# Performance work log

Measured on AMD Instinct MI355X. Metric: run time of the kernel, lower is better.

The kernel has to match this reference:

```python
import jax, jax.numpy as jnp
import numpy as np

N_ENT, N_REL, N_TRIG, N_ARGS = 100000, 250000, 50000, 250000
ENT_DIM, REL_R, RTYPE_DIM, ROLE_DIM, REL_SIZE = 288, 256, 32, 256, 200
ARG_DIM = REL_R + RTYPE_DIM + ENT_DIM  # 576


def setup_inputs() -> dict:
    key = jax.random.key(0)
    ks = jax.random.split(key, 11)
    s_in = 1.0 / np.sqrt(ARG_DIM)
    return {
        "ent_embeds": jax.random.normal(ks[0], (N_ENT, ENT_DIM), jnp.float32),
        "rel_embeds": jax.random.normal(ks[1], (N_REL, REL_R), jnp.float32),
        "rtype_table": jax.random.normal(ks[2], (REL_SIZE + 1, RTYPE_DIM), jnp.float32),
        "W_in": jax.random.normal(ks[3], (ARG_DIM, ROLE_DIM), jnp.float32) * s_in,
        "W_out": jax.random.normal(ks[4], (ARG_DIM, ROLE_DIM), jnp.float32) * s_in,
        "rtype_ids": jax.random.randint(ks[5], (N_REL,), 0, REL_SIZE, jnp.int32),
        "trig_ent_id": jax.random.randint(ks[6], (N_TRIG,), 0, N_ENT, jnp.int32),
        "arg_trig": jax.random.randint(ks[7], (N_ARGS,), 0, N_TRIG, jnp.int32),
        "arg_rel": jax.random.randint(ks[8], (N_ARGS,), 0, N_REL, jnp.int32),
        "arg_ent": jax.random.randint(ks[9], (N_ARGS,), 0, N_ENT, jnp.int32),
        "arg_is_in": jax.random.randint(ks[10], (N_ARGS,), 0, 2, jnp.int32),
    }


def reference(ent_embeds, rel_embeds, rtype_table, W_in, W_out,
              rtype_ids, trig_ent_id, arg_trig, arg_rel, arg_ent, arg_is_in):
    # per-relation type embedding (rtype_embedding_layer)
    rt_embeds = rtype_table[rtype_ids]                       # [N_REL, RTYPE_DIM]
    # per-argument gather + concat (get_arg_embeds): [rel | rtype | arg-entity]
    x = jnp.concatenate([rel_embeds[arg_rel],
                         rt_embeds[arg_rel],
                         ent_embeds[arg_ent]], axis=-1)      # [N_ARGS, ARG_DIM]
    # in_arg_layer vs out_arg_layer selected per argument (io_ids membership)
    m = arg_is_in.astype(x.dtype)[:, None]
    y = (x * m) @ W_in + (x * (1.0 - m)) @ W_out             # [N_ARGS, ROLE_DIM]
    # sum-aggregate per trigger (torch.sum over stacked arg embeds)
    args_sum = jax.ops.segment_sum(y, arg_trig, num_segments=N_TRIG)
    # concat trigger embedding with aggregated args (event_representation)
    return jnp.concatenate([ent_embeds[trig_ent_id], args_sum], axis=-1)  # [N_TRIG, ENT_DIM+ROLE_DIM]
```

## Files before the change

kernel.cpp:

```cpp
#include <hip/hip_runtime.h>
#include <hip/hip_bf16.h>
#include <stdint.h>

#define N_ENT    100000
#define N_REL    250000
#define N_TRIG   50000
#define N_ARGS   250000
#define ENT_DIM  288
#define REL_R    256
#define RTYPE_DIM 32
#define ROLE_DIM 256
#define ARG_DIM  576
#define OUT_DIM  544

#define BM 64
#define BK 32
#define NSTEP (ARG_DIM / BK)
#define LDP 40
#define CSP 258

typedef __attribute__((ext_vector_type(8))) short bf16x8;
typedef __attribute__((ext_vector_type(4))) short bf16x4;
typedef __attribute__((ext_vector_type(4))) float f32x4;

__device__ __forceinline__ short f2b(float f) {
    union { float f; uint32_t u; } v; v.f = f;
    uint32_t u = v.u;
    uint32_t r = (u + 0x7fffu + ((u >> 16) & 1u)) >> 16;
    return (short)r;
}

__global__ void __launch_bounds__(256)
k_init(const float* __restrict__ ent, const int* __restrict__ trig_ent,
       float* __restrict__ out)
{
    const int t    = blockIdx.x * 4 + (threadIdx.x >> 6);
    const int lane = threadIdx.x & 63;
    const int e    = trig_ent[t];
    const float4* src = (const float4*)(ent + (size_t)e * ENT_DIM);
    float4*       dst = (float4*)(out + (size_t)t * OUT_DIM);
    const float4 z = {0.f, 0.f, 0.f, 0.f};
    dst[lane] = src[lane];
    if (lane < 8) dst[64 + lane] = src[64 + lane];
    dst[72 + lane] = z;
}

__global__ void __launch_bounds__(256)
k_prep(const float* __restrict__ W_in, const float* __restrict__ W_out,
       short* __restrict__ Wb)
{
    const int idx = blockIdx.x * 256 + threadIdx.x;
    const int w   = idx / (ARG_DIM * ROLE_DIM);
    const int rem = idx % (ARG_DIM * ROLE_DIM);
    const int k   = rem / ROLE_DIM;
    const int col = rem % ROLE_DIM;
    const float* src = (w == 0) ? W_in : W_out;
    Wb[((size_t)w * ROLE_DIM + col) * ARG_DIM + k] = f2b(src[k * ROLE_DIM + col]);
}

__global__ void __launch_bounds__(256)
k_hist(const int* __restrict__ arg_trig, int* __restrict__ cnt)
{
    const int a = blockIdx.x * 256 + threadIdx.x;
    if (a < N_ARGS) atomicAdd(&cnt[arg_trig[a]], 1);
}

#define SCAN_T 1024
#define SCAN_B ((N_TRIG + SCAN_T - 1) / SCAN_T)

__global__ void __launch_bounds__(SCAN_T)
k_scan1(const int* __restrict__ cnt, int* __restrict__ off,
        int* __restrict__ bsum)
{
    __shared__ int buf[SCAN_T];
    const int tid = threadIdx.x;
    const int i   = blockIdx.x * SCAN_T + tid;
    int v = (i < N_TRIG) ? cnt[i] : 0;
    buf[tid] = v;
    __syncthreads();
#pragma unroll
    for (int o = 1; o < SCAN_T; o <<= 1) {
        int x = (tid >= o) ? buf[tid - o] : 0;
        __syncthreads();
        buf[tid] += x;
        __syncthreads();
    }
    if (i < N_TRIG) off[i] = buf[tid] - v;
    if (tid == SCAN_T - 1) bsum[blockIdx.x] = buf[tid];
}

__global__ void __launch_bounds__(64)
k_scan2(int* __restrict__ bsum)
{
    if (threadIdx.x == 0) {
        int s = 0;
        for (int i = 0; i < SCAN_B; ++i) { int t = bsum[i]; bsum[i] = s; s += t; }
    }
}

__global__ void __launch_bounds__(SCAN_T)
k_scan3(int* __restrict__ off, const int* __restrict__ bsum)
{
    const int i = blockIdx.x * SCAN_T + threadIdx.x;
    if (i < N_TRIG) off[i] += bsum[blockIdx.x];
}

__global__ void __launch_bounds__(256)
k_scatter(const int* __restrict__ arg_trig, const int* __restrict__ off,
          int* __restrict__ cur, int* __restrict__ idx)
{
    const int a = blockIdx.x * 256 + threadIdx.x;
    if (a < N_ARGS) {
        const int t = arg_trig[a];
        const int p = atomicAdd(&cur[t], 1);
        idx[off[t] + p] = a;
    }
}

__global__ void __launch_bounds__(512, 4)
k_gemm(const float* __restrict__ ent,  const float* __restrict__ rel,
       const float* __restrict__ rtab, const short* __restrict__ Wb,
       const int* __restrict__ rtype_ids, const int* __restrict__ arg_trig,
       const int* __restrict__ arg_rel,   const int* __restrict__ arg_ent,
       const int* __restrict__ arg_is_in, const int* __restrict__ idx,
       float* __restrict__ out)
{
    __shared__ short As[2][BM][LDP];
    __shared__ float Cs[BM][CSP];
    __shared__ int s_rel[BM], s_ent[BM], s_rt[BM], s_trig[BM], s_mask[BM];

    const int tid = threadIdx.x;
    const int a0  = blockIdx.x * BM;

    if (tid < BM) {
        int i     = a0 + tid;
        int valid = (i < N_ARGS);
        int a     = idx[valid ? i : (N_ARGS - 1)];
        int r     = arg_rel[a];
        s_rel[tid]  = r;
        s_ent[tid]  = arg_ent[a];
        s_rt[tid]   = rtype_ids[r];
        s_trig[tid] = valid ? arg_trig[a] : -1;
        s_mask[tid] = valid ? arg_is_in[a] : -1;
    }
    __syncthreads();

    const int lane  = tid & 63;
    const int wave  = tid >> 6;
    const int quad  = lane >> 4;
    const int l15   = lane & 15;
    const int nbase = wave * 32;

    const int srow = tid >> 3;
    const int skq  = (tid & 7) * 4;

    const float* p_rel = rel  + (size_t)s_rel[srow] * REL_R    + skq;
    const float* p_rt  = rtab + s_rt[srow] * RTYPE_DIM         + skq;
    const float* p_ent = ent  + (size_t)s_ent[srow] * ENT_DIM  + skq;

    const short* wbl = Wb + (size_t)(nbase + l15) * ARG_DIM + quad * 8;

    int rowmask[4];
#pragma unroll
    for (int m = 0; m < 4; ++m) rowmask[m] = s_mask[m * 16 + l15];

    f32x4 acc[4][2];
#pragma unroll
    for (int m = 0; m < 4; ++m)
#pragma unroll
        for (int n = 0; n < 2; ++n) acc[m][n] = (f32x4){0.f, 0.f, 0.f, 0.f};

    const bf16x8 zf = {0, 0, 0, 0, 0, 0, 0, 0};

    float4 vA = *(const float4*)(p_rel);
    float4 vB = *(const float4*)(p_rel + BK);
    float4 vC = *(const float4*)(p_rel + 2 * BK);

    auto STEP = [&](int s, float4& w) {
        bf16x4 h;
        h[0] = f2b(w.x); h[1] = f2b(w.y); h[2] = f2b(w.z); h[3] = f2b(w.w);
        *(bf16x4*)&As[s & 1][srow][skq] = h;

        asm volatile("s_waitcnt lgkmcnt(0)" ::: "memory");
        __builtin_amdgcn_s_barrier();
        asm volatile("" ::: "memory");

        bf16x8 a[4];
#pragma unroll
        for (int m = 0; m < 4; ++m)
            a[m] = *(const bf16x8*)&As[s & 1][m * 16 + l15][quad * 8];

        const short* bp = wbl + s * BK;
        const bf16x8 bi0 = *(const bf16x8*)(bp);
        const bf16x8 bi1 = *(const bf16x8*)(bp + 16 * ARG_DIM);
        const bf16x8 bo0 = *(const bf16x8*)(bp + (size_t)ROLE_DIM * ARG_DIM);
        const bf16x8 bo1 = *(const bf16x8*)(bp + (size_t)(ROLE_DIM + 16) * ARG_DIM);

#pragma unroll
        for (int m = 0; m < 4; ++m) {
            const bf16x8 ain = (rowmask[m] == 1) ? a[m] : zf;
            const bf16x8 aot = (rowmask[m] == 0) ? a[m] : zf;
            acc[m][0] = __builtin_amdgcn_mfma_f32_16x16x32_bf16(ain, bi0, acc[m][0], 0, 0, 0);
            acc[m][0] = __builtin_amdgcn_mfma_f32_16x16x32_bf16(aot, bo0, acc[m][0], 0, 0, 0);
            acc[m][1] = __builtin_amdgcn_mfma_f32_16x16x32_bf16(ain, bi1, acc[m][1], 0, 0, 0);
            acc[m][1] = __builtin_amdgcn_mfma_f32_16x16x32_bf16(aot, bo1, acc[m][1], 0, 0, 0);
        }

        __builtin_amdgcn_sched_barrier(0);
        if (s + 3 < NSTEP) {
            const int sn = s + 3;
            const float* src = (sn < 8)  ? (p_rel + sn * BK)
                             : (sn == 8) ? p_rt
                                         : (p_ent + (sn - 9) * BK);
            w = *(const float4*)src;
        }
    };

#pragma unroll
    for (int ss = 0; ss < NSTEP; ss += 3) {
        STEP(ss,     vA);
        STEP(ss + 1, vB);
        STEP(ss + 2, vC);
    }

#pragma unroll
    for (int m = 0; m < 4; ++m)
#pragma unroll
        for (int n = 0; n < 2; ++n)
#pragma unroll
            for (int r4 = 0; r4 < 4; ++r4)
                Cs[m * 16 + quad * 4 + r4][nbase + n * 16 + l15] = acc[m][n][r4];
    __syncthreads();

    {
        const int c    = tid & 255;
        const int half = tid >> 8;
        const int r0   = half * 32;
        const int rend = r0 + 32;

        int   runTrig  = s_trig[r0];
        int   runStart = r0;
        float sum      = 0.f;
        for (int r = r0; r < rend; ++r) {
            const int t = s_trig[r];
            if (t != runTrig) {
                if (runTrig >= 0) {
                    float* p = out + (size_t)runTrig * OUT_DIM + ENT_DIM + c;
                    if (runStart == r0) atomicAdd(p, sum);
                    else                *p = sum;
                }
                runTrig = t; runStart = r; sum = 0.f;
            }
            sum += Cs[r][c];
        }
        if (runTrig >= 0) {
            float* p = out + (size_t)runTrig * OUT_DIM + ENT_DIM + c;
            atomicAdd(p, sum);
        }
    }
}

extern "C" void kernel_launch(void* const* d_in, const int* in_sizes, int n_in,
                              void* d_out, int out_size, void* d_ws, size_t ws_size,
                              hipStream_t stream)
{
    const float* ent      = (const float*)d_in[0];
    const float* rel      = (const float*)d_in[1];
    const float* rtab     = (const float*)d_in[2];
    const float* W_in     = (const float*)d_in[3];
    const float* W_out    = (const float*)d_in[4];
    const int*  rtype_ids = (const int*)d_in[5];
    const int*  trig_ent  = (const int*)d_in[6];
    const int*  arg_trig  = (const int*)d_in[7];
    const int*  arg_rel   = (const int*)d_in[8];
    const int*  arg_ent   = (const int*)d_in[9];
    const int*  arg_is_in = (const int*)d_in[10];

    float* out = (float*)d_out;

    char* ws   = (char*)d_ws;
    short* Wb  = (short*)(ws);
    int*   cnt = (int*)(ws + 589824);
    int*   cur = (int*)(ws + 789824);
    int*   off = (int*)(ws + 989824);
    int*   bsum= (int*)(ws + 1190080);
    int*   idx = (int*)(ws + 1190400);

    hipMemsetAsync(cnt, 0, 400000, stream);

    hipLaunchKernelGGL(k_init, dim3(N_TRIG / 4), dim3(256), 0, stream,
                       ent, trig_ent, out);
    hipLaunchKernelGGL(k_prep, dim3(2 * ARG_DIM * ROLE_DIM / 256), dim3(256), 0,
                       stream, W_in, W_out, Wb);
    hipLaunchKernelGGL(k_hist, dim3((N_ARGS + 255) / 256), dim3(256), 0, stream,
                       arg_trig, cnt);
    hipLaunchKernelGGL(k_scan1, dim3(SCAN_B), dim3(SCAN_T), 0, stream,
                       cnt, off, bsum);
    hipLaunchKernelGGL(k_scan2, dim3(1), dim3(64), 0, stream, bsum);
    hipLaunchKernelGGL(k_scan3, dim3(SCAN_B), dim3(SCAN_T), 0, stream,
                       off, bsum);
    hipLaunchKernelGGL(k_scatter, dim3((N_ARGS + 255) / 256), dim3(256), 0,
                       stream, arg_trig, off, cur, idx);
    hipLaunchKernelGGL(k_gemm, dim3((N_ARGS + BM - 1) / BM), dim3(512), 0, stream,
                       ent, rel, rtab, Wb,
                       rtype_ids, arg_trig, arg_rel, arg_ent, arg_is_in, idx, out);
}
```

Before: 801.5 us.

## Stage full A tile in LDS upfront and merge the small prep/scan launches

```diff
diff --git a/kernel.cpp b/kernel.cpp
--- a/kernel.cpp
+++ b/kernel.cpp
@@ -16,7 +16,7 @@
 #define BM 64
 #define BK 32
 #define NSTEP (ARG_DIM / BK)
-#define LDP 40
+#define LDPK 584
 #define CSP 258
 
 typedef __attribute__((ext_vector_type(8))) short bf16x8;
@@ -46,23 +46,20 @@
 }
 
 __global__ void __launch_bounds__(256)
-k_prep(const float* __restrict__ W_in, const float* __restrict__ W_out,
-       short* __restrict__ Wb)
+k_prep_hist(const float* __restrict__ W_in, const float* __restrict__ W_out,
+            short* __restrict__ Wb,
+            const int* __restrict__ arg_trig, int* __restrict__ cnt)
 {
     const int idx = blockIdx.x * 256 + threadIdx.x;
-    const int w   = idx / (ARG_DIM * ROLE_DIM);
-    const int rem = idx % (ARG_DIM * ROLE_DIM);
-    const int k   = rem / ROLE_DIM;
-    const int col = rem % ROLE_DIM;
-    const float* src = (w == 0) ? W_in : W_out;
-    Wb[((size_t)w * ROLE_DIM + col) * ARG_DIM + k] = f2b(src[k * ROLE_DIM + col]);
-}
-
-__global__ void __launch_bounds__(256)
-k_hist(const int* __restrict__ arg_trig, int* __restrict__ cnt)
-{
-    const int a = blockIdx.x * 256 + threadIdx.x;
-    if (a < N_ARGS) atomicAdd(&cnt[arg_trig[a]], 1);
+    {
+        const int w   = idx / (ARG_DIM * ROLE_DIM);
+        const int rem = idx % (ARG_DIM * ROLE_DIM);
+        const int k   = rem / ROLE_DIM;
+        const int col = rem % ROLE_DIM;
+        const float* src = (w == 0) ? W_in : W_out;
+        Wb[((size_t)w * ROLE_DIM + col) * ARG_DIM + k] = f2b(src[k * ROLE_DIM + col]);
+    }
+    if (idx < N_ARGS) atomicAdd(&cnt[arg_trig[idx]], 1);
 }
 
 #define SCAN_T 1024
@@ -89,31 +86,28 @@
     if (tid == SCAN_T - 1) bsum[blockIdx.x] = buf[tid];
 }
 
-__global__ void __launch_bounds__(64)
-k_scan2(int* __restrict__ bsum)
-{
+__global__ void __launch_bounds__(SCAN_T)
+k_scan3(int* __restrict__ off, const int* __restrict__ bsum)
+{
+    __shared__ int sh;
     if (threadIdx.x == 0) {
         int s = 0;
-        for (int i = 0; i < SCAN_B; ++i) { int t = bsum[i]; bsum[i] = s; s += t; }
-    }
-}
-
-__global__ void __launch_bounds__(SCAN_T)
-k_scan3(int* __restrict__ off, const int* __restrict__ bsum)
-{
+        for (int j = 0; j < (int)blockIdx.x; ++j) s += bsum[j];
+        sh = s;
+    }
+    __syncthreads();
     const int i = blockIdx.x * SCAN_T + threadIdx.x;
-    if (i < N_TRIG) off[i] += bsum[blockIdx.x];
+    if (i < N_TRIG) off[i] += sh;
 }
 
 __global__ void __launch_bounds__(256)
-k_scatter(const int* __restrict__ arg_trig, const int* __restrict__ off,
-          int* __restrict__ cur, int* __restrict__ idx)
+k_scatter(const int* __restrict__ arg_trig, int* __restrict__ off,
+          int* __restrict__ idx)
 {
     const int a = blockIdx.x * 256 + threadIdx.x;
     if (a < N_ARGS) {
-        const int t = arg_trig[a];
-        const int p = atomicAdd(&cur[t], 1);
-        idx[off[t] + p] = a;
+        const int p = atomicAdd(&off[arg_trig[a]], 1);
+        idx[p] = a;
     }
 }
 
@@ -125,8 +119,7 @@
        const int* __restrict__ arg_is_in, const int* __restrict__ idx,
        float* __restrict__ out)
 {
-    __shared__ short As[2][BM][LDP];
-    __shared__ float Cs[BM][CSP];
+    __shared__ alignas(16) short As[BM][LDPK];
     __shared__ int s_rel[BM], s_ent[BM], s_rt[BM], s_trig[BM], s_mask[BM];
 
     const int tid = threadIdx.x;
@@ -158,43 +151,59 @@
     const float* p_rt  = rtab + s_rt[srow] * RTYPE_DIM         + skq;
     const float* p_ent = ent  + (size_t)s_ent[srow] * ENT_DIM  + skq;
 
+    {
+        float4 t[9];
+#pragma unroll
+        for (int s = 0; s < 8; ++s) t[s] = *(const float4*)(p_rel + s * BK);
+        t[8] = *(const float4*)p_rt;
+#pragma unroll
+        for (int s = 0; s < 9; ++s) {
+            bf16x4 h;
+            h[0] = f2b(t[s].x); h[1] = f2b(t[s].y);
+            h[2] = f2b(t[s].z); h[3] = f2b(t[s].w);
+            *(bf16x4*)&As[srow][s * BK + skq] = h;
+        }
+    }
+    {
+        float4 t[9];
+#pragma unroll
+        for (int s = 0; s < 9; ++s) t[s] = *(const float4*)(p_ent + s * BK);
+#pragma unroll
+        for (int s = 0; s < 9; ++s) {
+            bf16x4 h;
+            h[0] = f2b(t[s].x); h[1] = f2b(t[s].y);
+            h[2] = f2b(t[s].z); h[3] = f2b(t[s].w);
+            *(bf16x4*)&As[srow][(s + 9) * BK + skq] = h;
+        }
+    }
+
+    int rowmask[4];
+#pragma unroll
+    for (int m = 0; m < 4; ++m) rowmask[m] = s_mask[m * 16 + l15];
+
+    f32x4 acc[4][2];
+#pragma unroll
+    for (int m = 0; m < 4; ++m)
+#pragma unroll
+        for (int n = 0; n < 2; ++n) acc[m][n] = (f32x4){0.f, 0.f, 0.f, 0.f};
+
     const short* wbl = Wb + (size_t)(nbase + l15) * ARG_DIM + quad * 8;
-
-    int rowmask[4];
-#pragma unroll
-    for (int m = 0; m < 4; ++m) rowmask[m] = s_mask[m * 16 + l15];
-
-    f32x4 acc[4][2];
-#pragma unroll
-    for (int m = 0; m < 4; ++m)
-#pragma unroll
-        for (int n = 0; n < 2; ++n) acc[m][n] = (f32x4){0.f, 0.f, 0.f, 0.f};
-
     const bf16x8 zf = {0, 0, 0, 0, 0, 0, 0, 0};
 
-    float4 vA = *(const float4*)(p_rel);
-    float4 vB = *(const float4*)(p_rel + BK);
-    float4 vC = *(const float4*)(p_rel + 2 * BK);
-
-    auto STEP = [&](int s, float4& w) {
-        bf16x4 h;
-        h[0] = f2b(w.x); h[1] = f2b(w.y); h[2] = f2b(w.z); h[3] = f2b(w.w);
-        *(bf16x4*)&As[s & 1][srow][skq] = h;
-
-        asm volatile("s_waitcnt lgkmcnt(0)" ::: "memory");
-        __builtin_amdgcn_s_barrier();
-        asm volatile("" ::: "memory");
-
-        bf16x8 a[4];
-#pragma unroll
-        for (int m = 0; m < 4; ++m)
-            a[m] = *(const bf16x8*)&As[s & 1][m * 16 + l15][quad * 8];
-
+    __syncthreads();
+
+#pragma unroll
+    for (int s = 0; s < NSTEP; ++s) {
         const short* bp = wbl + s * BK;
         const bf16x8 bi0 = *(const bf16x8*)(bp);
         const bf16x8 bi1 = *(const bf16x8*)(bp + 16 * ARG_DIM);
         const bf16x8 bo0 = *(const bf16x8*)(bp + (size_t)ROLE_DIM * ARG_DIM);
         const bf16x8 bo1 = *(const bf16x8*)(bp + (size_t)(ROLE_DIM + 16) * ARG_DIM);
+
+        bf16x8 a[4];
+#pragma unroll
+        for (int m = 0; m < 4; ++m)
+            a[m] = *(const bf16x8*)&As[m * 16 + l15][s * BK + quad * 8];
 
 #pragma unroll
         for (int m = 0; m < 4; ++m) {
@@ -205,24 +214,10 @@
             acc[m][1] = __builtin_amdgcn_mfma_f32_16x16x32_bf16(ain, bi1, acc[m][1], 0, 0, 0);
             acc[m][1] = __builtin_amdgcn_mfma_f32_16x16x32_bf16(aot, bo1, acc[m][1], 0, 0, 0);
         }
-
-        __builtin_amdgcn_sched_barrier(0);
-        if (s + 3 < NSTEP) {
-            const int sn = s + 3;
-            const float* src = (sn < 8)  ? (p_rel + sn * BK)
-                             : (sn == 8) ? p_rt
-                                         : (p_ent + (sn - 9) * BK);
-            w = *(const float4*)src;
-        }
-    };
-
-#pragma unroll
-    for (int ss = 0; ss < NSTEP; ss += 3) {
-        STEP(ss,     vA);
-        STEP(ss + 1, vB);
-        STEP(ss + 2, vC);
-    }
-
+    }
+
+    __syncthreads();
+    float (*Cs)[CSP] = (float(*)[CSP])&As[0][0];
 #pragma unroll
     for (int m = 0; m < 4; ++m)
 #pragma unroll
@@ -281,26 +276,22 @@
     char* ws   = (char*)d_ws;
     short* Wb  = (short*)(ws);
     int*   cnt = (int*)(ws + 589824);
-    int*   cur = (int*)(ws + 789824);
-    int*   off = (int*)(ws + 989824);
-    int*   bsum= (int*)(ws + 1190080);
-    int*   idx = (int*)(ws + 1190400);
-
-    hipMemsetAsync(cnt, 0, 400000, stream);
+    int*   off = (int*)(ws + 789824);
+    int*   bsum= (int*)(ws + 989824);
+    int*   idx = (int*)(ws + 990080);
+
+    hipMemsetAsync(cnt, 0, 200000, stream);
 
     hipLaunchKernelGGL(k_init, dim3(N_TRIG / 4), dim3(256), 0, stream,
                        ent, trig_ent, out);
-    hipLaunchKernelGGL(k_prep, dim3(2 * ARG_DIM * ROLE_DIM / 256), dim3(256), 0,
-                       stream, W_in, W_out, Wb);
-    hipLaunchKernelGGL(k_hist, dim3((N_ARGS + 255) / 256), dim3(256), 0, stream,
-                       arg_trig, cnt);
+    hipLaunchKernelGGL(k_prep_hist, dim3(2 * ARG_DIM * ROLE_DIM / 256), dim3(256),
+                       0, stream, W_in, W_out, Wb, arg_trig, cnt);
     hipLaunchKernelGGL(k_scan1, dim3(SCAN_B), dim3(SCAN_T), 0, stream,
                        cnt, off, bsum);
-    hipLaunchKernelGGL(k_scan2, dim3(1), dim3(64), 0, stream, bsum);
     hipLaunchKernelGGL(k_scan3, dim3(SCAN_B), dim3(SCAN_T), 0, stream,
                        off, bsum);
     hipLaunchKernelGGL(k_scatter, dim3((N_ARGS + 255) / 256), dim3(256), 0,
-                       stream, arg_trig, off, cur, idx);
+                       stream, arg_trig, off, idx);
     hipLaunchKernelGGL(k_gemm, dim3((N_ARGS + BM - 1) / BM), dim3(512), 0, stream,
                        ent, rel, rtab, Wb,
                        rtype_ids, arg_trig, arg_rel, arg_ent, arg_is_in, idx, out);
```

New measurement: 755.4 us. -5.8%, faster.
